# Performance work log

Measured on AMD Instinct MI355X. Metric: run time of the kernel, lower is better.

## Reference

```python
import jax, jax.numpy as jnp
import numpy as np

B, T, D, H = 2, 1024, 1024, 16
K = D            # key_dim = hidden * expand_k (1.0)
V = 2 * D        # value_dim = hidden * expand_v (2.0)
DK, DV = K // H, V // H
I = 2816         # SwiGLU intermediate
CONV = 4
EPS = 1e-6


def rmsnorm(x, w, eps=EPS):
    return x * jax.lax.rsqrt(jnp.mean(x * x, -1, keepdims=True) + eps) * w


def l2norm(x, eps=EPS):
    return x * jax.lax.rsqrt(jnp.sum(x * x, -1, keepdims=True) + eps)


def short_conv(x, w):
    # depthwise causal conv1d (kernel CONV, no bias) + silu; x [B,T,C], w [C,CONV]
    kern = w.T[:, None, :]  # [CONV, 1, C]
    y = jax.lax.conv_general_dilated(
        x, kern, (1,), [(CONV - 1, 0)],
        dimension_numbers=('NWC', 'WIO', 'NWC'),
        feature_group_count=x.shape[-1])
    return jax.nn.silu(y)


def setup_inputs() -> dict:
    key = jax.random.key(0)
    ks = jax.random.split(key, 20)
    p = lambda i, shape, s=0.02: jax.random.normal(ks[i], shape, jnp.float32) * s
    return dict(
        x=jax.random.normal(ks[0], (B, T, D), jnp.float32),
        norm1_w=jnp.ones((D,), jnp.float32),
        wq=p(1, (D, K)), wk=p(2, (D, K)), wv=p(3, (D, V)),
        conv_q=p(4, (K, CONV), 0.3), conv_k=p(5, (K, CONV), 0.3), conv_v=p(6, (V, CONV), 0.3),
        wb=p(7, (D, H)), wa=p(8, (D, H)),
        A_log=jnp.log(jax.random.uniform(ks[9], (H,), jnp.float32, 1.0, 16.0)),
        dt_bias=jnp.log(jnp.expm1(jax.random.uniform(ks[10], (H,), jnp.float32, 0.001, 0.1))),
        wg=p(11, (D, V)),
        o_norm_w=jnp.ones((DV,), jnp.float32),
        wo=p(12, (V, D)),
        norm2_w=jnp.ones((D,), jnp.float32),
        w1=p(13, (D, I)), w2=p(14, (I, D)), w3=p(15, (D, I)),
    )


def reference(x, norm1_w, wq, wk, wv, conv_q, conv_k, conv_v, wb, wa,
              A_log, dt_bias, wg, o_norm_w, wo, norm2_w, w1, w2, w3):
    h = rmsnorm(x, norm1_w)
    # projections + short causal conv (silu)
    q = short_conv(h @ wq, conv_q).reshape(B, T, H, DK)
    k = short_conv(h @ wk, conv_k).reshape(B, T, H, DK)
    v = short_conv(h @ wv, conv_v).reshape(B, T, H, DV)
    q = l2norm(q) * (DK ** -0.5)
    k = l2norm(k)
    beta = jax.nn.sigmoid(h @ wb)                              # [B,T,H]
    # mamba-style decay gate: g = -exp(A_log) * softplus(a + dt_bias)
    g = -jnp.exp(A_log) * jax.nn.softplus(h @ wa + dt_bias)   # [B,T,H]

    # gated delta rule: S_t = exp(g_t)*S_{t-1}; u_t = beta_t*(v_t - k_t^T S_t);
    # S_t += k_t u_t^T; o_t = q_t^T S_t
    def step(S, inp):
        qt, kt, vt, gt, bt = inp                               # [B,H,*]
        S = S * jnp.exp(gt)[..., None, None]
        u = (vt - jnp.einsum('bhk,bhkv->bhv', kt, S)) * bt[..., None]
        S = S + kt[..., None] * u[:, :, None, :]
        ot = jnp.einsum('bhk,bhkv->bhv', qt, S)
        return S, ot

    S0 = jnp.zeros((B, H, DK, DV), x.dtype)
    seq = (q.transpose(1, 0, 2, 3), k.transpose(1, 0, 2, 3),
           v.transpose(1, 0, 2, 3), g.transpose(1, 0, 2), beta.transpose(1, 0, 2))
    _, o = jax.lax.scan(step, S0, seq)
    o = o.transpose(1, 0, 2, 3)                                # [B,T,H,DV]

    # output gate: per-head RMSNorm * swish(gate), then out-projection
    gate = (h @ wg).reshape(B, T, H, DV)
    o = rmsnorm(o, o_norm_w) * gate * jax.nn.sigmoid(gate)
    x = x + o.reshape(B, T, V) @ wo

    # SwiGLU MLP with residual
    h2 = rmsnorm(x, norm2_w)
    return x + (jax.nn.silu(h2 @ w1) * (h2 @ w3)) @ w2
```

## Files before the change

kernel.cpp:

```cpp
#include <hip/hip_runtime.h>
#include <stdint.h>

typedef unsigned short u16;
typedef float f32x4 __attribute__((ext_vector_type(4)));
typedef __bf16 bf16x8 __attribute__((ext_vector_type(8)));
typedef unsigned short u16x8 __attribute__((ext_vector_type(8)));

#define N1P 6400

__device__ __forceinline__ u16 f2bf(float f) {
    union { float f; uint32_t u; } v; v.f = f;
    uint32_t u = v.u;
    return (u16)((u + 0x7FFFu + ((u >> 16) & 1u)) >> 16);
}
__device__ __forceinline__ float bf2f(u16 h) {
    union { uint32_t u; float f; } v; v.u = ((uint32_t)h) << 16; return v.f;
}
__device__ __forceinline__ float sigm(float x) { return 1.f / (1.f + __expf(-x)); }

__device__ __forceinline__ void async16(const u16* g, u16* l) {
    __builtin_amdgcn_global_load_lds((const __attribute__((address_space(1))) void*)g,
                                     (__attribute__((address_space(3))) void*)l, 16, 0, 0);
}

__device__ __forceinline__ int swz64(int row, int col) {
    return row * 128 + ((((col >> 3) ^ (row & 7)) << 3) + (col & 7)) * 2;
}
__device__ __forceinline__ bf16x8 frag64(const u16* m, int rowbase, int lane, int kk) {
    const int row = rowbase + (lane & 15);
    const int unit = (lane >> 4) + (kk << 2);
    return *(const bf16x8*)((const char*)m + row * 128 + ((unit ^ (row & 7)) << 4));
}

struct TJob { const float* src; u16* dst; int rows, cols, rowOff, rowStride, nOut, blkBase, gx, mode; };
struct TJobs { TJob j[10]; };

__global__ __launch_bounds__(256) void k_transpose_all(TJobs jobs, int njobs) {
    __shared__ float tile[64][33];
    const int bid = blockIdx.x;
    int ji = 0;
#pragma unroll
    for (int i = 1; i < 10; ++i)
        if (i < njobs && bid >= jobs.j[i].blkBase) ji = i;
    const TJob J = jobs.j[ji];
    const int bx = bid - J.blkBase;
    const int n0 = (bx % J.gx) * 32, k0 = (bx / J.gx) * 64;
    const int tid = threadIdx.x;
    const int tx = tid & 31, ty = tid >> 5;
    const int c = n0 + tx;
    const bool cok = (c < J.cols);
#pragma unroll
    for (int i = 0; i < 8; ++i) {
        const int r = k0 + i * 8 + ty;
        tile[i * 8 + ty][tx] = cok ? J.src[(size_t)r * J.cols + c] : 0.f;
    }
    __syncthreads();
    const int n = tid >> 3, seg = tid & 7;
    const int ng = n0 + n;
    if (ng < J.nOut) {
        u16x8 o;
#pragma unroll
        for (int e = 0; e < 8; ++e) o[e] = f2bf(tile[seg * 8 + e][n]);
        const int drow = (J.mode == 0) ? (J.rowOff + ng * J.rowStride)
                                       : (J.rowOff + ((ng >> 4) << 5) + (ng & 15));
        *(u16x8*)&J.dst[(size_t)drow * J.rows + k0 + seg * 8] = o;
    }
}

__global__ __launch_bounds__(256) void k_rmsnorm(const float* __restrict__ x, const float* __restrict__ w,
                                                 u16* __restrict__ out) {
    const int row = blockIdx.x, tid = threadIdx.x, lane = tid & 63, wave = tid >> 6;
    const float4 v = ((const float4*)(x + (size_t)row * 1024))[tid];
    float ss = v.x * v.x + v.y * v.y + v.z * v.z + v.w * v.w;
#pragma unroll
    for (int o = 1; o < 64; o <<= 1) ss += __shfl_xor(ss, o);
    __shared__ float sred[4];
    if (lane == 0) sred[wave] = ss;
    __syncthreads();
    const float tot = sred[0] + sred[1] + sred[2] + sred[3];
    const float rn = rsqrtf(tot * (1.f / 1024.f) + 1e-6f);
    const float4 wv = ((const float4*)w)[tid];
    uint2 pk;
    pk.x = (uint32_t)f2bf(v.x * rn * wv.x) | ((uint32_t)f2bf(v.y * rn * wv.y) << 16);
    pk.y = (uint32_t)f2bf(v.z * rn * wv.z) | ((uint32_t)f2bf(v.w * rn * wv.w) << 16);
    *(uint2*)&out[(size_t)row * 1024 + tid * 4] = pk;
}

template <int EPI>
__global__ __launch_bounds__(512, 2) void k_gemm256(const u16* __restrict__ A, const u16* __restrict__ Bt,
                                                    u16* __restrict__ Cout, int N, int Kd) {
    __shared__ __align__(16) u16 L[65536];
    const int q8 = (int)gridDim.x >> 3;
    const int bid = blockIdx.x;
    const int wg = (bid & 7) * q8 + (bid >> 3);
    const int bm = wg & 7, bn = wg >> 3;
    const int tid = threadIdx.x, lane = tid & 63, wave = tid >> 6;
    const int wm = wave >> 2, wn = wave & 3;

    const int scol = ((tid & 7) ^ ((tid >> 3) & 7)) * 8;
    const u16* gA = A + (size_t)(bm * 256 + (tid >> 3)) * Kd + scol;
    const u16* gB = Bt + (size_t)(bn * 256 + (tid >> 3)) * Kd + scol;
    u16* dstT = L + tid * 8;

    const int NT = Kd >> 6;
    const int NI = NT >> 1;

    auto issue = [&](const u16* g, int mtx, int kt, int h) {
        u16* d = dstT + (kt & 1) * 32768 + mtx * 16384 + h * 8192;
        const u16* s = g + (size_t)(h * 128) * Kd + kt * 64;
        async16(s, d);
        async16(s + (size_t)64 * Kd, d + 4096);
    };

    issue(gB, 1, 0, 0); issue(gB, 1, 0, 1);
    issue(gA, 0, 0, 0); issue(gA, 0, 0, 1);
    issue(gB, 1, 1, 0); issue(gB, 1, 1, 1);
    asm volatile("s_waitcnt vmcnt(4)" ::: "memory");
    __builtin_amdgcn_s_barrier();

    f32x4 acc[8][4] = {};
    bf16x8 bq[4][2];

    for (int i = 0; i < NI; ++i) {
        const int kt0 = 2 * i;
#pragma unroll
        for (int p = 0; p < 8; ++p) {
            const int half = p >> 2;
            const int q = p & 3;
            const u16* Ab = L + half * 32768;
            const u16* Bb = L + half * 32768 + 16384;
            if (q == 0) {
#pragma unroll
                for (int ni = 0; ni < 4; ++ni)
#pragma unroll
                    for (int kk = 0; kk < 2; ++kk)
                        bq[ni][kk] = frag64(Bb, wn * 64 + ni * 16, lane, kk);
            }
            bf16x8 af[2][2];
#pragma unroll
            for (int j = 0; j < 2; ++j)
#pragma unroll
                for (int kk = 0; kk < 2; ++kk)
                    af[j][kk] = frag64(Ab, wm * 128 + (2 * q + j) * 16, lane, kk);
            if (p == 0) { if (kt0 + 1 < NT) issue(gA, 0, kt0 + 1, 0); }
            if (p == 1) { if (kt0 + 1 < NT) issue(gA, 0, kt0 + 1, 1);
                          if (kt0 + 2 < NT) issue(gB, 1, kt0 + 2, 0); }
            if (p == 2) { if (kt0 + 2 < NT) issue(gB, 1, kt0 + 2, 1); }
            if (p == 4) { if (kt0 + 2 < NT) issue(gA, 0, kt0 + 2, 0); }
            if (p == 5) { if (kt0 + 2 < NT) issue(gA, 0, kt0 + 2, 1);
                          if (kt0 + 3 < NT) issue(gB, 1, kt0 + 3, 0); }
            if (p == 6) { if (kt0 + 3 < NT) issue(gB, 1, kt0 + 3, 1); }
            if (p == 3) { if (i + 1 < NI) { asm volatile("s_waitcnt vmcnt(4)" ::: "memory"); }
                          else            { asm volatile("s_waitcnt vmcnt(0)" ::: "memory"); } }
            if (p == 7) { if (i + 1 < NI) { asm volatile("s_waitcnt vmcnt(4)" ::: "memory"); } }
            __builtin_amdgcn_s_barrier();
            __builtin_amdgcn_s_setprio(1);
#pragma unroll
            for (int j = 0; j < 2; ++j)
#pragma unroll
                for (int ni = 0; ni < 4; ++ni)
#pragma unroll
                    for (int kk = 0; kk < 2; ++kk)
                        acc[2 * q + j][ni] = __builtin_amdgcn_mfma_f32_16x16x32_bf16(
                            af[j][kk], bq[ni][kk], acc[2 * q + j][ni], 0, 0, 0);
            __builtin_amdgcn_s_setprio(0);
            __builtin_amdgcn_s_barrier();
        }
    }

    const int rsub = (lane >> 4) * 4, csub = lane & 15;
    if constexpr (EPI == 2) {
        u16* ct = L;
#pragma unroll
        for (int r = 0; r < 2; ++r) {
            if (wm == r) {
#pragma unroll
                for (int mi = 0; mi < 8; ++mi)
#pragma unroll
                    for (int ni = 0; ni < 4; ++ni)
#pragma unroll
                        for (int rr = 0; rr < 4; ++rr)
                            ct[(mi * 16 + rsub + rr) * 264 + wn * 64 + ni * 16 + csub] =
                                f2bf(acc[mi][ni][rr]);
            }
            __syncthreads();
#pragma unroll
            for (int k = 0; k < 8; ++k) {
                const int f = (tid + k * 512) * 8;
                const int r2 = f >> 8, c = f & 255;
                *(u16x8*)&Cout[(size_t)(bm * 256 + r * 128 + r2) * N + bn * 256 + c] =
                    *(const u16x8*)&ct[r2 * 264 + c];
            }
            __syncthreads();
        }
    } else {
        u16* ct = L;
#pragma unroll
        for (int mi = 0; mi < 8; ++mi)
#pragma unroll
            for (int g = 0; g < 2; ++g)
#pragma unroll
                for (int rr = 0; rr < 4; ++rr) {
                    const float u1 = acc[mi][2 * g][rr];
                    const float u3 = acc[mi][2 * g + 1][rr];
                    ct[(wm * 128 + mi * 16 + rsub + rr) * 132 + wn * 32 + g * 16 + csub] =
                        f2bf(u1 * sigm(u1) * u3);
                }
        __syncthreads();
#pragma unroll
        for (int k = 0; k < 8; ++k) {
            const int f = (tid + k * 512) * 8;
            const int r2 = f >> 7, c = f & 127;
            *(u16x8*)&Cout[(size_t)(bm * 256 + r2) * N + bn * 128 + c] =
                *(const u16x8*)&ct[r2 * 132 + c];
        }
    }
}

__global__ __launch_bounds__(512) void k_gemm_skinny(const u16* __restrict__ A, const u16* __restrict__ Bt,
                                                     float* __restrict__ Cout, const float* __restrict__ Res,
                                                     int N, int Kd) {
    __shared__ __align__(16) char smem[49152];
    u16* Asb = (u16*)smem;
    u16* Bsb = (u16*)(smem + 32768);
    const int q = (int)gridDim.x >> 3;
    const int bid = blockIdx.x;
    const int wg = (bid & 7) * q + (bid >> 3);
    const int bm = wg & 15, bn = wg >> 4;
    const int tid = threadIdx.x, lane = tid & 63, wave = tid >> 6;
    const int wm = wave >> 1, wn = wave & 1;

    const int srow = tid >> 3;
    const int scol = ((tid & 7) ^ ((tid >> 3) & 7)) * 8;
    const u16* gA = A + (size_t)(bm * 128 + srow) * Kd + scol;
    const u16* gB = Bt + (size_t)(bn * 64 + srow) * Kd + scol;

    f32x4 acc[2][2] = {};
    const int NT = Kd >> 6;

    async16(gA, Asb + wave * 512);
    async16(gA + (size_t)64 * Kd, Asb + 4096 + wave * 512);
    async16(gB, Bsb + wave * 512);
    asm volatile("s_waitcnt vmcnt(0)" ::: "memory");
    __syncthreads();

    int buf = 0;
    for (int t = 0; t < NT; ++t) {
        if (t + 1 < NT) {
            const int k0 = (t + 1) << 6;
            const int ba = (buf ^ 1) * 8192, bb2 = (buf ^ 1) * 4096;
            async16(gA + k0, Asb + ba + wave * 512);
            async16(gA + (size_t)64 * Kd + k0, Asb + ba + 4096 + wave * 512);
            async16(gB + k0, Bsb + bb2 + wave * 512);
        }
        const u16* Ab = Asb + buf * 8192;
        const u16* Bb = Bsb + buf * 4096;
#pragma unroll
        for (int kk = 0; kk < 2; ++kk) {
            bf16x8 af[2], bfr[2];
#pragma unroll
            for (int mi = 0; mi < 2; ++mi) af[mi] = frag64(Ab, wm * 32 + mi * 16, lane, kk);
#pragma unroll
            for (int ni = 0; ni < 2; ++ni) bfr[ni] = frag64(Bb, wn * 32 + ni * 16, lane, kk);
#pragma unroll
            for (int mi = 0; mi < 2; ++mi)
#pragma unroll
                for (int ni = 0; ni < 2; ++ni)
                    acc[mi][ni] = __builtin_amdgcn_mfma_f32_16x16x32_bf16(af[mi], bfr[ni], acc[mi][ni], 0, 0, 0);
        }
        asm volatile("s_waitcnt vmcnt(0)" ::: "memory");
        __syncthreads();
        buf ^= 1;
    }

    const int rsub = (lane >> 4) * 4;
    const int csub = lane & 15;
    float* ctile = (float*)smem;
#pragma unroll
    for (int mi = 0; mi < 2; ++mi)
#pragma unroll
        for (int ni = 0; ni < 2; ++ni)
#pragma unroll
            for (int r = 0; r < 4; ++r)
                ctile[(wm * 32 + mi * 16 + rsub + r) * 68 + wn * 32 + ni * 16 + csub] = acc[mi][ni][r];
    __syncthreads();
#pragma unroll
    for (int k = 0; k < 4; ++k) {
        const int f = (tid + k * 512) * 4;
        const int r = f >> 6, c = f & 63;
        float4 v = *(const float4*)&ctile[r * 68 + c];
        const float4 rv = *(const float4*)&Res[(size_t)(bm * 128 + r) * N + bn * 64 + c];
        v.x += rv.x; v.y += rv.y; v.z += rv.z; v.w += rv.w;
        *(float4*)&Cout[(size_t)(bm * 128 + r) * N + bn * 64 + c] = v;
    }
}

__global__ __launch_bounds__(256) void k_conv(const u16* __restrict__ P, const float* __restrict__ cwq,
                                              const float* __restrict__ cwk, const float* __restrict__ cwv,
                                              const float* __restrict__ A_log, const float* __restrict__ dtb,
                                              u16* __restrict__ Qb, u16* __restrict__ Kb,
                                              u16* __restrict__ Vb, float* __restrict__ Gl,
                                              float* __restrict__ Bbuf) {
    const int bid = blockIdx.x;
    const int row = (bid & 7) * 256 + (bid >> 3);
    const int t = row & 1023;
    const int tid = threadIdx.x;
    const long prow = (long)row * N1P;
#pragma unroll
    for (int p = 0; p < 2; ++p) {
        const int g = p * 256 + tid;
        const int c = g * 8;
        u16x8 taps[4];
#pragma unroll
        for (int j = 0; j < 4; ++j) {
            const int tt = t - 3 + j;
            if (tt >= 0) taps[j] = *(const u16x8*)&P[prow + (long)(j - 3) * N1P + c];
            else         taps[j] = u16x8{};
        }
        const float* cw = (c < 1024) ? (cwq + c * 4)
                          : (c < 2048) ? (cwk + (c - 1024) * 4)
                                       : (cwv + (c - 2048) * 4);
        float y[8];
#pragma unroll
        for (int e = 0; e < 8; ++e) {
            const float4 w = ((const float4*)cw)[e];
            float v = bf2f(taps[0][e]) * w.x + bf2f(taps[1][e]) * w.y +
                      bf2f(taps[2][e]) * w.z + bf2f(taps[3][e]) * w.w;
            y[e] = v * sigm(v);
        }
        if (c < 2048) {
            float ss = 0.f;
#pragma unroll
            for (int e = 0; e < 8; ++e) ss += y[e] * y[e];
            ss += __shfl_xor(ss, 1); ss += __shfl_xor(ss, 2); ss += __shfl_xor(ss, 4);
            const float rn = rsqrtf(ss + 1e-6f);
            const float sc = (c < 1024) ? rn * 0.125f : rn;
            u16x8 o;
#pragma unroll
            for (int e = 0; e < 8; ++e) o[e] = f2bf(y[e] * sc);
            if (c < 1024) *(u16x8*)&Qb[(size_t)row * 1024 + c] = o;
            else          *(u16x8*)&Kb[(size_t)row * 1024 + (c - 1024)] = o;
        } else {
            u16x8 o;
#pragma unroll
            for (int e = 0; e < 8; ++e) o[e] = f2bf(y[e]);
            *(u16x8*)&Vb[(size_t)row * 2048 + (c - 2048)] = o;
        }
    }
    if (tid < 32) {
        const int h = tid & 15;
        const float val = bf2f(P[prow + 4096 + tid]);
        if (tid < 16) {
            Bbuf[(size_t)row * 16 + h] = sigm(val);
        } else {
            const float a = val + dtb[h];
            const float sp = (a > 15.f) ? a : log1pf(__expf(a));
            Gl[(size_t)row * 16 + h] = -__expf(A_log[h]) * sp;
        }
    }
}

__global__ __launch_bounds__(256) void k_scan1(
    const u16* __restrict__ Qb, const u16* __restrict__ Kb, const u16* __restrict__ Vb,
    const float* __restrict__ Gl, const float* __restrict__ Bb,
    u16* __restrict__ CHW, u16* __restrict__ CHM, u16* __restrict__ CHQc,
    u16* __restrict__ CHKcT, u16* __restrict__ CHU0T, float* __restrict__ CHcC,
    u16* __restrict__ CHA2m, u16* __restrict__ CHB) {
    __shared__ __align__(16) char sm[66048];
    u16* Ql   = (u16*)(sm);
    u16* Kl   = (u16*)(sm + 8192);
    u16* VTb  = (u16*)(sm + 16384);
    u16* KT1b = (u16*)(sm + 32768);
    u16* Mim  = (u16*)(sm + 40960);
    u16* MTim = (u16*)(sm + 49152);
    u16* Tb   = (u16*)(sm + 57344);
    float* Tl    = (float*)sm;
    float* gcs   = (float*)(sm + 65536);
    float* betal = (float*)(sm + 65792);

    const int blk = blockIdx.x;
    const int bb = blk >> 8, h = (blk >> 4) & 15, ch = blk & 15;
    const int bhc = blk;
    const int tid = threadIdx.x, lane = tid & 63, wave = tid >> 6;
    const long rowbase = (long)bb * 1024 + ch * 64;

    if (tid < 64) {
        gcs[tid] = Gl[(rowbase + tid) * 16 + h];
        betal[tid] = Bb[(rowbase + tid) * 16 + h];
    }
    for (int u = tid; u < 512; u += 256) {
        int r = u >> 3, c8 = u & 7;
        uint4 kv = *(const uint4*)&Kb[(rowbase + r) * 1024 + h * 64 + c8 * 8];
        uint4 qv = *(const uint4*)&Qb[(rowbase + r) * 1024 + h * 64 + c8 * 8];
        int b = r * 128 + ((c8 ^ (r & 7)) << 4);
        *(uint4*)((char*)Kl + b) = kv;
        *(uint4*)((char*)Ql + b) = qv;
    }
    __syncthreads();
    if (wave == 0) {
        float g = gcs[lane];
#pragma unroll
        for (int off = 1; off < 64; off <<= 1) {
            float n = __shfl_up(g, off, 64);
            if (lane >= off) g += n;
        }
        gcs[lane] = g;
    }
    for (int u = tid; u < 1024; u += 256) {
        int r = u >> 4, c8 = u & 15;
        u16x8 vv = *(const u16x8*)&Vb[(rowbase + r) * 2048 + h * 128 + c8 * 8];
        float bsc = betal[r];
#pragma unroll
        for (int j = 0; j < 8; ++j) {
            int dv = c8 * 8 + j;
            *(u16*)((char*)VTb + swz64(dv, r)) = f2bf(bf2f(vv[j]) * bsc);
        }
    }
    f32x4 aQK[4] = {}, aKK[4] = {};
#pragma unroll
    for (int nt = 0; nt < 4; ++nt)
#pragma unroll
        for (int kk = 0; kk < 2; ++kk) {
            bf16x8 bq = frag64(Kl, nt * 16, lane, kk);
            aQK[nt] = __builtin_amdgcn_mfma_f32_16x16x32_bf16(frag64(Ql, wave * 16, lane, kk), bq, aQK[nt], 0, 0, 0);
            aKK[nt] = __builtin_amdgcn_mfma_f32_16x16x32_bf16(frag64(Kl, wave * 16, lane, kk), bq, aKK[nt], 0, 0, 0);
        }
    __syncthreads();

    const float gcsC = gcs[63];
    float am[4][4];
#pragma unroll
    for (int nt = 0; nt < 4; ++nt)
#pragma unroll
        for (int reg = 0; reg < 4; ++reg) {
            int t = wave * 16 + ((lane >> 4) << 2) + reg;
            int i = nt * 16 + (lane & 15);
            float dec = __expf(gcs[t] - gcs[i]);
            float mv = (i <= t) ? dec * aQK[nt][reg] : 0.f;
            *(u16*)((char*)CHM + (size_t)bhc * 8192 + swz64(t, i)) = f2bf(mv);
            float a = (i < t) ? betal[t] * dec * aKK[nt][reg] : 0.f;
            am[nt][reg] = -a;
            u16 amb = f2bf(-a);
            *(u16*)((char*)Mim + swz64(t, i)) = amb;
            *(u16*)((char*)MTim + swz64(i, t)) = amb;
        }
    for (int e = tid; e < 4096; e += 256) {
        int r = e >> 6, c = e & 63;
        int ib = swz64(r, c);
        float qv = bf2f(*(const u16*)((const char*)Ql + ib)) * __expf(gcs[r]);
        *(u16*)((char*)CHQc + (size_t)bhc * 8192 + ib) = f2bf(qv);
        float kv = bf2f(*(const u16*)((const char*)Kl + ib));
        int ob = swz64(c, r);
        *(u16*)((char*)KT1b + ob) = f2bf(kv * betal[r] * __expf(gcs[r]));
        *(u16*)((char*)CHKcT + (size_t)bhc * 8192 + ob) = f2bf(kv * __expf(gcsC - gcs[r]));
    }
    if (tid == 0) CHcC[bhc] = __expf(gcsC);
    __syncthreads();

#pragma unroll
    for (int nt = 0; nt < 4; ++nt)
#pragma unroll
        for (int reg = 0; reg < 4; ++reg) {
            int t = wave * 16 + ((lane >> 4) << 2) + reg;
            int i = nt * 16 + (lane & 15);
            float tv = (t == i) ? 1.f : am[nt][reg];
            Tl[t * 64 + i] = tv;
            *(u16*)((char*)Tb + swz64(t, i)) = f2bf(tv);
        }
    __syncthreads();

    const int hi = wave * 16 + 15;
#pragma unroll
    for (int j = 1; j <= 5; ++j) {
        f32x4 aM[4] = {};
#pragma unroll
        for (int nt = 0; nt < 4; ++nt) {
            if (nt * 16 > hi - (1 << j)) continue;
#pragma unroll
            for (int kk = 0; kk < 2; ++kk) {
                if (kk * 32 > hi) break;
                aM[nt] = __builtin_amdgcn_mfma_f32_16x16x32_bf16(
                    frag64(Mim, wave * 16, lane, kk), frag64(MTim, nt * 16, lane, kk), aM[nt], 0, 0, 0);
            }
        }
        __syncthreads();
#pragma unroll
        for (int nt = 0; nt < 4; ++nt)
#pragma unroll
            for (int reg = 0; reg < 4; ++reg) {
                int t = wave * 16 + ((lane >> 4) << 2) + reg;
                int i = nt * 16 + (lane & 15);
                float mv = (t - i >= (1 << j)) ? aM[nt][reg] : 0.f;
                u16 mb = f2bf(mv);
                *(u16*)((char*)Mim + swz64(t, i)) = mb;
                *(u16*)((char*)MTim + swz64(i, t)) = mb;
            }
        __syncthreads();
        f32x4 aT[4];
#pragma unroll
        for (int nt = 0; nt < 4; ++nt)
#pragma unroll
            for (int reg = 0; reg < 4; ++reg) {
                int t = wave * 16 + ((lane >> 4) << 2) + reg;
                int i = nt * 16 + (lane & 15);
                aT[nt][reg] = Tl[t * 64 + i];
            }
#pragma unroll
        for (int nt = 0; nt < 4; ++nt) {
            if (nt * 16 > hi - (1 << j)) continue;
#pragma unroll
            for (int kk = 0; kk < 2; ++kk) {
                if (kk * 32 > hi) break;
                aT[nt] = __builtin_amdgcn_mfma_f32_16x16x32_bf16(
                    frag64(Tb, wave * 16, lane, kk), frag64(MTim, nt * 16, lane, kk), aT[nt], 0, 0, 0);
            }
        }
#pragma unroll
        for (int nt = 0; nt < 4; ++nt)
#pragma unroll
            for (int reg = 0; reg < 4; ++reg) {
                int t = wave * 16 + ((lane >> 4) << 2) + reg;
                int i = nt * 16 + (lane & 15);
                Tl[t * 64 + i] = aT[nt][reg];
                *(u16*)((char*)Tb + swz64(t, i)) = f2bf(aT[nt][reg]);
            }
    }
    __syncthreads();

    u16* KcTl = Ql;
    u16* WTl  = Kl;
    u16* U0Tl = Mim;
#pragma unroll
    for (int r = 0; r < 2; ++r) {
        const int g = r * 256 + tid;
        async16(CHKcT + (size_t)bhc * 4096 + (size_t)g * 8, KcTl + g * 8);
    }

    {
        f32x4 aW[4] = {};
#pragma unroll
        for (int nt = 0; nt < 4; ++nt)
#pragma unroll
            for (int kk = 0; kk < 2; ++kk) {
                if (kk * 32 > hi) break;
                aW[nt] = __builtin_amdgcn_mfma_f32_16x16x32_bf16(
                    frag64(Tb, wave * 16, lane, kk), frag64(KT1b, nt * 16, lane, kk), aW[nt], 0, 0, 0);
            }
#pragma unroll
        for (int nt = 0; nt < 4; ++nt)
#pragma unroll
            for (int reg = 0; reg < 4; ++reg) {
                int r = wave * 16 + ((lane >> 4) << 2) + reg;
                int c = nt * 16 + (lane & 15);
                u16 wv = f2bf(aW[nt][reg]);
                *(u16*)((char*)CHW + (size_t)bhc * 8192 + swz64(r, c)) = wv;
                *(u16*)((char*)WTl + swz64(c, r)) = wv;
            }
    }
#pragma unroll
    for (int rt = 0; rt < 2; ++rt) {
        f32x4 aU[4] = {};
        int rb = (wave * 2 + rt) * 16;
#pragma unroll
        for (int nt = 0; nt < 4; ++nt)
#pragma unroll
            for (int kk = 0; kk < 2; ++kk) {
                if (kk * 32 > nt * 16 + 15) continue;
                aU[nt] = __builtin_amdgcn_mfma_f32_16x16x32_bf16(
                    frag64(VTb, rb, lane, kk), frag64(Tb, nt * 16, lane, kk), aU[nt], 0, 0, 0);
            }
#pragma unroll
        for (int nt = 0; nt < 4; ++nt)
#pragma unroll
            for (int reg = 0; reg < 4; ++reg) {
                int dv = rb + ((lane >> 4) << 2) + reg;
                int c = nt * 16 + (lane & 15);
                u16 uv = f2bf(aU[nt][reg]);
                *(u16*)((char*)CHU0T + (size_t)bhc * 16384 + swz64(dv, c)) = uv;
                *(u16*)((char*)U0Tl + swz64(dv, c)) = uv;
            }
    }
    asm volatile("s_waitcnt vmcnt(0)" ::: "memory");
    __syncthreads();

    {
        f32x4 aA[4] = {};
#pragma unroll
        for (int nt = 0; nt < 4; ++nt)
#pragma unroll
            for (int kk = 0; kk < 2; ++kk)
                aA[nt] = __builtin_amdgcn_mfma_f32_16x16x32_bf16(
                    frag64(WTl, wave * 16, lane, kk), frag64(KcTl, nt * 16, lane, kk), aA[nt], 0, 0, 0);
#pragma unroll
        for (int nt = 0; nt < 4; ++nt)
#pragma unroll
            for (int reg = 0; reg < 4; ++reg) {
                int kI = wave * 16 + ((lane >> 4) << 2) + reg;
                int dk = nt * 16 + (lane & 15);
                *(u16*)((char*)CHA2m + (size_t)bhc * 8192 + swz64(dk, kI)) = f2bf(-aA[nt][reg]);
            }
    }
#pragma unroll
    for (int rt = 0; rt < 2; ++rt) {
        f32x4 aB[4] = {};
        int rb = (wave * 2 + rt) * 16;
#pragma unroll
        for (int nt = 0; nt < 4; ++nt)
#pragma unroll
            for (int kk = 0; kk < 2; ++kk)
                aB[nt] = __builtin_amdgcn_mfma_f32_16x16x32_bf16(
                    frag64(U0Tl, rb, lane, kk), frag64(KcTl, nt * 16, lane, kk), aB[nt], 0, 0, 0);
#pragma unroll
        for (int nt = 0; nt < 4; ++nt)
#pragma unroll
            for (int reg = 0; reg < 4; ++reg) {
                int dv = rb + ((lane >> 4) << 2) + reg;
                int dk = nt * 16 + (lane & 15);
                *(u16*)((char*)CHB + (size_t)bhc * 16384 + swz64(dv, dk)) = f2bf(aB[nt][reg]);
            }
    }
}

__global__ __launch_bounds__(256) void k_scan2(
    const u16* __restrict__ CHA2m, const u16* __restrict__ CHB,
    const float* __restrict__ CHcC, u16* __restrict__ CHS0) {
    __shared__ __align__(16) u16 stg[2][8192];
    __shared__ __align__(16) u16 STb[4096];
    __shared__ float ST[64 * 66];
    const int blk = blockIdx.x;
    const int bb = blk >> 5, h = (blk >> 1) & 15, dvh = blk & 1;
    const int bh = bb * 16 + h;
    const int tid = threadIdx.x, lane = tid & 63, wave = tid >> 6;

    for (int e = tid; e < 64 * 66; e += 256) ST[e] = 0.f;
    for (int e = tid; e < 4096; e += 256) STb[e] = 0;

    auto stage = [&](int buf, int ch) {
        const size_t base = (size_t)(bh * 16 + ch);
        const u16* sA = CHA2m + base * 4096;
        const u16* sB = CHB + base * 8192 + dvh * 4096;
#pragma unroll
        for (int r = 0; r < 2; ++r) {
            const int g = r * 256 + tid;
            async16(sA + (size_t)g * 8, &stg[buf][g * 8]);
            async16(sB + (size_t)g * 8, &stg[buf][4096 + g * 8]);
        }
    };
    stage(0, 0);
    int cur = 0;
    for (int ch = 0; ch < 16; ++ch) {
        asm volatile("s_waitcnt vmcnt(0)" ::: "memory");
        __syncthreads();
        if (ch < 15) stage(cur ^ 1, ch + 1);
        const u16* sA2 = &stg[cur][0];
        const u16* sB = &stg[cur][4096];
        f32x4 acc[4] = {};
#pragma unroll
        for (int nt = 0; nt < 4; ++nt)
#pragma unroll
            for (int kk = 0; kk < 2; ++kk)
                acc[nt] = __builtin_amdgcn_mfma_f32_16x16x32_bf16(
                    frag64(STb, wave * 16, lane, kk), frag64(sA2, nt * 16, lane, kk), acc[nt], 0, 0, 0);
        const float cC = CHcC[bh * 16 + ch];
        const size_t sbase = ((size_t)(bh * 16 + ch + 1) * 2 + dvh) * 8192;
#pragma unroll
        for (int nt = 0; nt < 4; ++nt)
#pragma unroll
            for (int reg = 0; reg < 4; ++reg) {
                const int rr = wave * 16 + ((lane >> 4) << 2) + reg;
                const int cc = nt * 16 + (lane & 15);
                const float bv = bf2f(*(const u16*)((const char*)sB + swz64(rr, cc)));
                const float ns = cC * ST[rr * 66 + cc] + acc[nt][reg] + bv;
                ST[rr * 66 + cc] = ns;
                const u16 nb = f2bf(ns);
                *(u16*)((char*)STb + swz64(rr, cc)) = nb;
                if (ch < 15) *(u16*)((char*)CHS0 + sbase + swz64(rr, cc)) = nb;
            }
        cur ^= 1;
    }
}

__global__ __launch_bounds__(256) void k_scan3(
    const u16* __restrict__ CHM, const u16* __restrict__ CHQc, const u16* __restrict__ CHW,
    const u16* __restrict__ CHU0T, const u16* __restrict__ CHS0, const u16* __restrict__ P,
    const float* __restrict__ onw, u16* __restrict__ OG) {
    __shared__ __align__(16) char sm3[73728];
    u16* sM  = (u16*)sm3;
    u16* sQc = (u16*)(sm3 + 8192);
    u16* sW  = (u16*)(sm3 + 16384);
    u16* sU  = (u16*)(sm3 + 24576);
    u16* sS0 = (u16*)(sm3 + 40960);
    u16* sPg = (u16*)(sm3 + 57344);
    const int blk = blockIdx.x;
    const int bb = blk >> 8, h = (blk >> 4) & 15, ch = blk & 15;
    const size_t bhc = blk;
    const int tid = threadIdx.x, lane = tid & 63, wave = tid >> 6;
    const bool hasS0 = (ch != 0);

#pragma unroll
    for (int r = 0; r < 2; ++r) {
        const int g = r * 256 + tid;
        async16(CHM + bhc * 4096 + (size_t)g * 8, sM + g * 8);
        async16(CHQc + bhc * 4096 + (size_t)g * 8, sQc + g * 8);
        async16(CHW + bhc * 4096 + (size_t)g * 8, sW + g * 8);
#pragma unroll
        for (int d = 0; d < 2; ++d) {
            async16(CHU0T + (bhc * 2 + d) * 4096 + (size_t)g * 8, sU + d * 4096 + g * 8);
            if (hasS0)
                async16(CHS0 + (bhc * 2 + d) * 4096 + (size_t)g * 8, sS0 + d * 4096 + g * 8);
        }
    }
    const long prow0 = ((long)bb * 1024 + ch * 64) * N1P + 4128 + h * 128;
#pragma unroll
    for (int k = 0; k < 4; ++k) {
        const int i = tid + k * 256;
        const int row = i >> 4, seg = i & 15;
        async16(P + prow0 + (long)row * N1P + seg * 8, sPg + i * 8);
    }
    asm volatile("s_waitcnt vmcnt(0)" ::: "memory");
    __syncthreads();

    if (hasS0) {
#pragma unroll
        for (int d = 0; d < 2; ++d) {
            f32x4 au[4] = {};
#pragma unroll
            for (int nt = 0; nt < 4; ++nt)
#pragma unroll
                for (int kk = 0; kk < 2; ++kk)
                    au[nt] = __builtin_amdgcn_mfma_f32_16x16x32_bf16(
                        frag64(sS0 + d * 4096, wave * 16, lane, kk), frag64(sW, nt * 16, lane, kk),
                        au[nt], 0, 0, 0);
#pragma unroll
            for (int nt = 0; nt < 4; ++nt)
#pragma unroll
                for (int reg = 0; reg < 4; ++reg) {
                    const int dv = wave * 16 + ((lane >> 4) << 2) + reg;
                    const int c = nt * 16 + (lane & 15);
                    u16* p = (u16*)((char*)sU + d * 8192 + swz64(dv, c));
                    *p = f2bf(bf2f(*p) - au[nt][reg]);
                }
        }
        __syncthreads();
    }

    f32x4 accO[2][4] = {};
#pragma unroll
    for (int d = 0; d < 2; ++d)
#pragma unroll
        for (int nt = 0; nt < 4; ++nt)
#pragma unroll
            for (int kk = 0; kk < 2; ++kk) {
                accO[d][nt] = __builtin_amdgcn_mfma_f32_16x16x32_bf16(
                    frag64(sM, wave * 16, lane, kk), frag64(sU + d * 4096, nt * 16, lane, kk),
                    accO[d][nt], 0, 0, 0);
                if (hasS0)
                    accO[d][nt] = __builtin_amdgcn_mfma_f32_16x16x32_bf16(
                        frag64(sQc, wave * 16, lane, kk), frag64(sS0 + d * 4096, nt * 16, lane, kk),
                        accO[d][nt], 0, 0, 0);
            }

    const int rsub = (lane >> 4) * 4, csub = lane & 15;
    float rn[4];
#pragma unroll
    for (int reg = 0; reg < 4; ++reg) {
        float ss = 0.f;
#pragma unroll
        for (int d = 0; d < 2; ++d)
#pragma unroll
            for (int nt = 0; nt < 4; ++nt) {
                const float v = accO[d][nt][reg];
                ss += v * v;
            }
        ss += __shfl_xor(ss, 1); ss += __shfl_xor(ss, 2);
        ss += __shfl_xor(ss, 4); ss += __shfl_xor(ss, 8);
        rn[reg] = rsqrtf(ss * (1.f / 128.f) + 1e-6f);
    }
    __syncthreads();
    u16* ct = (u16*)sm3;
#pragma unroll
    for (int d = 0; d < 2; ++d)
#pragma unroll
        for (int nt = 0; nt < 4; ++nt)
#pragma unroll
            for (int reg = 0; reg < 4; ++reg) {
                const int rr = wave * 16 + rsub + reg;
                const int dv = d * 64 + nt * 16 + csub;
                const float g = bf2f(sPg[rr * 128 + dv]);
                const float val = accO[d][nt][reg] * rn[reg] * onw[dv] * g * sigm(g);
                ct[rr * 136 + dv] = f2bf(val);
            }
    __syncthreads();
#pragma unroll
    for (int k = 0; k < 4; ++k) {
        const int f = (tid + k * 256) * 8;
        const int r2 = f >> 7, c = f & 127;
        *(u16x8*)&OG[(size_t)(bb * 1024 + ch * 64 + r2) * 2048 + h * 128 + c] =
            *(const u16x8*)&ct[r2 * 136 + c];
    }
}

extern "C" void kernel_launch(void* const* d_in, const int* in_sizes, int n_in,
                              void* d_out, int out_size, void* d_ws, size_t ws_size,
                              hipStream_t stream) {
    const float* x   = (const float*)d_in[0];
    const float* n1w = (const float*)d_in[1];
    const float* wq  = (const float*)d_in[2];
    const float* wk  = (const float*)d_in[3];
    const float* wv  = (const float*)d_in[4];
    const float* cq  = (const float*)d_in[5];
    const float* ck  = (const float*)d_in[6];
    const float* cv  = (const float*)d_in[7];
    const float* wb  = (const float*)d_in[8];
    const float* wa  = (const float*)d_in[9];
    const float* Alg = (const float*)d_in[10];
    const float* dtb = (const float*)d_in[11];
    const float* wg  = (const float*)d_in[12];
    const float* onw = (const float*)d_in[13];
    const float* wo  = (const float*)d_in[14];
    const float* n2w = (const float*)d_in[15];
    const float* w1  = (const float*)d_in[16];
    const float* w2  = (const float*)d_in[17];
    const float* w3  = (const float*)d_in[18];

    if (ws_size < 132384768ULL) return;

    char* ws = (char*)d_ws;
    u16*   WcatT = (u16*)(ws + 0);
    u16*   WoT   = (u16*)(ws + 13107200);
    u16*   W13T  = (u16*)(ws + 17301504);
    u16*   W2T   = (u16*)(ws + 28835840);
    u16*   hA    = (u16*)(ws + 34603008);
    u16*   P     = (u16*)(ws + 38797312);
    u16*   Qb    = (u16*)(ws + 65011712);
    u16*   Kb    = (u16*)(ws + 69206016);
    u16*   Vb    = (u16*)(ws + 73400320);
    float* Gl    = (float*)(ws + 81788928);
    float* Bbf   = (float*)(ws + 81920000);
    float* X2    = (float*)(ws + 82051072);
    u16*   CHKcT = (u16*)(ws + 98828288);
    u16*   CHU0T = (u16*)(ws + 103022592);
    float* CHcC  = (float*)(ws + 111411200);
    u16*   CHA2m = (u16*)(ws + 111413248);
    u16*   CHB   = (u16*)(ws + 115607552);
    u16*   CHS0  = (u16*)(ws + 123996160);
    u16*   CHW   = WcatT;
    u16*   CHM   = (u16*)(ws + 4194304);
    u16*   CHQc  = (u16*)(ws + 8388608);
    u16*   Mm  = Qb;
    u16*   OG  = Vb;
    u16*   h2A = hA;

    TJobs tj;
    tj.j[0] = { wq, WcatT, 1024, 1024,    0, 1, 1024,     0, 32, 0 };
    tj.j[1] = { wk, WcatT, 1024, 1024, 1024, 1, 1024,   512, 32, 0 };
    tj.j[2] = { wv, WcatT, 1024, 2048, 2048, 1, 2048,  1024, 64, 0 };
    tj.j[3] = { wb, WcatT, 1024,   16, 4096, 1,   16,  2048,  1, 0 };
    tj.j[4] = { wa, WcatT, 1024,   16, 4112, 1,   16,  2064,  1, 0 };
    tj.j[5] = { wg, WcatT, 1024, 2048, 4128, 1, 2272,  2080, 71, 0 };
    tj.j[6] = { wo, WoT,   2048, 1024,    0, 1, 1024,  3216, 32, 0 };
    tj.j[7] = { w1, W13T,  1024, 2816,    0, 1, 2816,  4240, 88, 1 };
    tj.j[8] = { w3, W13T,  1024, 2816,   16, 1, 2816,  5648, 88, 1 };
    tj.j[9] = { w2, W2T,   2816, 1024,    0, 1, 1024,  7056, 32, 0 };
    k_transpose_all<<<8464, 256, 0, stream>>>(tj, 10);

    k_rmsnorm<<<2048, 256, 0, stream>>>(x, n1w, hA);
    k_gemm256<2><<<200, 512, 0, stream>>>(hA, WcatT, P, N1P, 1024);

    k_conv<<<2048, 256, 0, stream>>>(P, cq, ck, cv, Alg, dtb, Qb, Kb, Vb, Gl, Bbf);

    k_scan1<<<512, 256, 0, stream>>>(Qb, Kb, Vb, Gl, Bbf, CHW, CHM, CHQc, CHKcT, CHU0T, CHcC,
                                     CHA2m, CHB);
    k_scan2<<<64, 256, 0, stream>>>(CHA2m, CHB, CHcC, CHS0);
    k_scan3<<<512, 256, 0, stream>>>(CHM, CHQc, CHW, CHU0T, CHS0, P, onw, OG);

    k_gemm_skinny<<<256, 512, 0, stream>>>(OG, WoT, X2, x, 1024, 2048);

    k_rmsnorm<<<2048, 256, 0, stream>>>(X2, n2w, h2A);
    k_gemm256<3><<<176, 512, 0, stream>>>(h2A, W13T, Mm, 2816, 1024);
    k_gemm_skinny<<<256, 512, 0, stream>>>(Mm, W2T, (float*)d_out, X2, 1024, 2816);
}
```

Baseline: 238.1 us.

## Fuse short conv, l2norm and gate computation into chunk scan kernel

```diff
diff --git a/kernel.cpp b/kernel.cpp
--- a/kernel.cpp
+++ b/kernel.cpp
@@ -295,74 +295,9 @@
     }
 }
 
-__global__ __launch_bounds__(256) void k_conv(const u16* __restrict__ P, const float* __restrict__ cwq,
-                                              const float* __restrict__ cwk, const float* __restrict__ cwv,
-                                              const float* __restrict__ A_log, const float* __restrict__ dtb,
-                                              u16* __restrict__ Qb, u16* __restrict__ Kb,
-                                              u16* __restrict__ Vb, float* __restrict__ Gl,
-                                              float* __restrict__ Bbuf) {
-    const int bid = blockIdx.x;
-    const int row = (bid & 7) * 256 + (bid >> 3);
-    const int t = row & 1023;
-    const int tid = threadIdx.x;
-    const long prow = (long)row * N1P;
-#pragma unroll
-    for (int p = 0; p < 2; ++p) {
-        const int g = p * 256 + tid;
-        const int c = g * 8;
-        u16x8 taps[4];
-#pragma unroll
-        for (int j = 0; j < 4; ++j) {
-            const int tt = t - 3 + j;
-            if (tt >= 0) taps[j] = *(const u16x8*)&P[prow + (long)(j - 3) * N1P + c];
-            else         taps[j] = u16x8{};
-        }
-        const float* cw = (c < 1024) ? (cwq + c * 4)
-                          : (c < 2048) ? (cwk + (c - 1024) * 4)
-                                       : (cwv + (c - 2048) * 4);
-        float y[8];
-#pragma unroll
-        for (int e = 0; e < 8; ++e) {
-            const float4 w = ((const float4*)cw)[e];
-            float v = bf2f(taps[0][e]) * w.x + bf2f(taps[1][e]) * w.y +
-                      bf2f(taps[2][e]) * w.z + bf2f(taps[3][e]) * w.w;
-            y[e] = v * sigm(v);
-        }
-        if (c < 2048) {
-            float ss = 0.f;
-#pragma unroll
-            for (int e = 0; e < 8; ++e) ss += y[e] * y[e];
-            ss += __shfl_xor(ss, 1); ss += __shfl_xor(ss, 2); ss += __shfl_xor(ss, 4);
-            const float rn = rsqrtf(ss + 1e-6f);
-            const float sc = (c < 1024) ? rn * 0.125f : rn;
-            u16x8 o;
-#pragma unroll
-            for (int e = 0; e < 8; ++e) o[e] = f2bf(y[e] * sc);
-            if (c < 1024) *(u16x8*)&Qb[(size_t)row * 1024 + c] = o;
-            else          *(u16x8*)&Kb[(size_t)row * 1024 + (c - 1024)] = o;
-        } else {
-            u16x8 o;
-#pragma unroll
-            for (int e = 0; e < 8; ++e) o[e] = f2bf(y[e]);
-            *(u16x8*)&Vb[(size_t)row * 2048 + (c - 2048)] = o;
-        }
-    }
-    if (tid < 32) {
-        const int h = tid & 15;
-        const float val = bf2f(P[prow + 4096 + tid]);
-        if (tid < 16) {
-            Bbuf[(size_t)row * 16 + h] = sigm(val);
-        } else {
-            const float a = val + dtb[h];
-            const float sp = (a > 15.f) ? a : log1pf(__expf(a));
-            Gl[(size_t)row * 16 + h] = -__expf(A_log[h]) * sp;
-        }
-    }
-}
-
 __global__ __launch_bounds__(256) void k_scan1(
-    const u16* __restrict__ Qb, const u16* __restrict__ Kb, const u16* __restrict__ Vb,
-    const float* __restrict__ Gl, const float* __restrict__ Bb,
+    const u16* __restrict__ P, const float* __restrict__ cwq, const float* __restrict__ cwk,
+    const float* __restrict__ cwv, const float* __restrict__ A_log, const float* __restrict__ dtb,
     u16* __restrict__ CHW, u16* __restrict__ CHM, u16* __restrict__ CHQc,
     u16* __restrict__ CHKcT, u16* __restrict__ CHU0T, float* __restrict__ CHcC,
     u16* __restrict__ CHA2m, u16* __restrict__ CHB) {
@@ -377,6 +312,7 @@
     float* Tl    = (float*)sm;
     float* gcs   = (float*)(sm + 65536);
     float* betal = (float*)(sm + 65792);
+    u16* Vtmp = Mim;
 
     const int blk = blockIdx.x;
     const int bb = blk >> 8, h = (blk >> 4) & 15, ch = blk & 15;
@@ -385,18 +321,57 @@
     const long rowbase = (long)bb * 1024 + ch * 64;
 
     if (tid < 64) {
-        gcs[tid] = Gl[(rowbase + tid) * 16 + h];
-        betal[tid] = Bb[(rowbase + tid) * 16 + h];
-    }
-    for (int u = tid; u < 512; u += 256) {
-        int r = u >> 3, c8 = u & 7;
-        uint4 kv = *(const uint4*)&Kb[(rowbase + r) * 1024 + h * 64 + c8 * 8];
-        uint4 qv = *(const uint4*)&Qb[(rowbase + r) * 1024 + h * 64 + c8 * 8];
-        int b = r * 128 + ((c8 ^ (r & 7)) << 4);
-        *(uint4*)((char*)Kl + b) = kv;
-        *(uint4*)((char*)Ql + b) = qv;
-    }
-    __syncthreads();
+        const long pr = (rowbase + tid) * (long)N1P;
+        betal[tid] = sigm(bf2f(P[pr + 4096 + h]));
+        const float a = bf2f(P[pr + 4112 + h]) + dtb[h];
+        const float sp = (a > 15.f) ? a : log1pf(__expf(a));
+        gcs[tid] = -__expf(A_log[h]) * sp;
+    }
+    {
+        const int g = tid & 31, rb2 = tid >> 5;
+        int colbase; const float* cw;
+        if (g < 8)       { const int cc = h * 64 + g * 8;        colbase = cc;        cw = cwq + cc * 4; }
+        else if (g < 16) { const int cc = h * 64 + (g - 8) * 8;   colbase = 1024 + cc; cw = cwk + cc * 4; }
+        else             { const int cc = h * 128 + (g - 16) * 8; colbase = 2048 + cc; cw = cwv + cc * 4; }
+        float4 wgt[8];
+#pragma unroll
+        for (int e = 0; e < 8; ++e) wgt[e] = ((const float4*)cw)[e];
+        u16x8 taps[11];
+#pragma unroll
+        for (int j = 0; j < 11; ++j) {
+            const int tloc = ch * 64 + rb2 * 8 - 3 + j;
+            if (tloc >= 0) taps[j] = *(const u16x8*)&P[((long)bb * 1024 + tloc) * N1P + colbase];
+            else           taps[j] = u16x8{};
+        }
+#pragma unroll
+        for (int r = 0; r < 8; ++r) {
+            float y[8];
+            float ss = 0.f;
+#pragma unroll
+            for (int e = 0; e < 8; ++e) {
+                float v = bf2f(taps[r][e]) * wgt[e].x + bf2f(taps[r + 1][e]) * wgt[e].y +
+                          bf2f(taps[r + 2][e]) * wgt[e].z + bf2f(taps[r + 3][e]) * wgt[e].w;
+                v = v * sigm(v);
+                y[e] = v;
+                ss += v * v;
+            }
+            ss += __shfl_xor(ss, 1); ss += __shfl_xor(ss, 2); ss += __shfl_xor(ss, 4);
+            const float rn = rsqrtf(ss + 1e-6f);
+            const float sc = (g < 8) ? rn * 0.125f : (g < 16 ? rn : 1.f);
+            u16x8 o;
+#pragma unroll
+            for (int e = 0; e < 8; ++e) o[e] = f2bf(y[e] * sc);
+            const int row = rb2 * 8 + r;
+            if (g < 16) {
+                u16* dst = (g < 8) ? Ql : Kl;
+                *(u16x8*)((char*)dst + row * 128 + (((g & 7) ^ (row & 7)) << 4)) = o;
+            } else {
+                *(u16x8*)&Vtmp[row * 128 + (g - 16) * 8] = o;
+            }
+        }
+    }
+    __syncthreads();
+
     if (wave == 0) {
         float g = gcs[lane];
 #pragma unroll
@@ -408,7 +383,7 @@
     }
     for (int u = tid; u < 1024; u += 256) {
         int r = u >> 4, c8 = u & 15;
-        u16x8 vv = *(const u16x8*)&Vb[(rowbase + r) * 2048 + h * 128 + c8 * 8];
+        u16x8 vv = *(const u16x8*)&Vtmp[r * 128 + c8 * 8];
         float bsc = betal[r];
 #pragma unroll
         for (int j = 0; j < 8; ++j) {
@@ -832,11 +807,8 @@
     u16*   W2T   = (u16*)(ws + 28835840);
     u16*   hA    = (u16*)(ws + 34603008);
     u16*   P     = (u16*)(ws + 38797312);
-    u16*   Qb    = (u16*)(ws + 65011712);
-    u16*   Kb    = (u16*)(ws + 69206016);
-    u16*   Vb    = (u16*)(ws + 73400320);
-    float* Gl    = (float*)(ws + 81788928);
-    float* Bbf   = (float*)(ws + 81920000);
+    u16*   Mm    = (u16*)(ws + 65011712);
+    u16*   OG    = (u16*)(ws + 73400320);
     float* X2    = (float*)(ws + 82051072);
     u16*   CHKcT = (u16*)(ws + 98828288);
     u16*   CHU0T = (u16*)(ws + 103022592);
@@ -847,8 +819,6 @@
     u16*   CHW   = WcatT;
     u16*   CHM   = (u16*)(ws + 4194304);
     u16*   CHQc  = (u16*)(ws + 8388608);
-    u16*   Mm  = Qb;
-    u16*   OG  = Vb;
     u16*   h2A = hA;
 
     TJobs tj;
@@ -867,10 +837,8 @@
     k_rmsnorm<<<2048, 256, 0, stream>>>(x, n1w, hA);
     k_gemm256<2><<<200, 512, 0, stream>>>(hA, WcatT, P, N1P, 1024);
 
-    k_conv<<<2048, 256, 0, stream>>>(P, cq, ck, cv, Alg, dtb, Qb, Kb, Vb, Gl, Bbf);
-
-    k_scan1<<<512, 256, 0, stream>>>(Qb, Kb, Vb, Gl, Bbf, CHW, CHM, CHQc, CHKcT, CHU0T, CHcC,
-                                     CHA2m, CHB);
+    k_scan1<<<512, 256, 0, stream>>>(P, cq, ck, cv, Alg, dtb, CHW, CHM, CHQc, CHKcT, CHU0T,
+                                     CHcC, CHA2m, CHB);
     k_scan2<<<64, 256, 0, stream>>>(CHA2m, CHB, CHcC, CHS0);
     k_scan3<<<512, 256, 0, stream>>>(CHM, CHQc, CHW, CHU0T, CHS0, P, onw, OG);
 
```

New measurement: 222.1 us. 1.07x faster.
